# Kernel optimization log

Measured on AMD Instinct MI355X. Metric: run time of the kernel, lower is better.

Reference implementation:

```python
import jax, jax.numpy as jnp
import numpy as np

N_NODES = 100000
N_EDGES = 320000
DIM = 256


def _graph_conv(src, dst, h, W, b):
    # DGL GraphConv, norm='both', in_feats == out_feats (aggregate-then-transform)
    ones = jnp.ones((src.shape[0],), dtype=h.dtype)
    out_deg = jnp.clip(jax.ops.segment_sum(ones, src, num_segments=N_NODES), 1.0)
    in_deg = jnp.clip(jax.ops.segment_sum(ones, dst, num_segments=N_NODES), 1.0)
    h = h * (out_deg ** -0.5)[:, None]          # src-side normalization
    agg = jax.ops.segment_sum(h[src], dst, num_segments=N_NODES)  # SpMM (copy_u, sum)
    agg = agg * (in_deg ** -0.5)[:, None]       # dst-side normalization
    return agg @ W + b


def setup_inputs() -> dict:
    key = jax.random.key(0)
    ks = jax.random.split(key, 7)
    src = jax.random.randint(ks[0], (N_EDGES,), 0, N_NODES, dtype=jnp.int32)
    dst = jax.random.randint(ks[1], (N_EDGES,), 0, N_NODES, dtype=jnp.int32)
    node_feature = jax.random.normal(ks[2], (N_NODES, DIM), dtype=jnp.float32)
    s = 1.0 / np.sqrt(DIM)
    W1 = jax.random.normal(ks[3], (DIM, DIM), dtype=jnp.float32) * s
    b1 = jnp.zeros((DIM,), dtype=jnp.float32)
    W2 = jax.random.normal(ks[4], (DIM, DIM), dtype=jnp.float32) * s
    b2 = jnp.zeros((DIM,), dtype=jnp.float32)
    return {"src": src, "dst": dst, "node_feature": node_feature,
            "W1": W1, "b1": b1, "W2": W2, "b2": b2}


def reference(src, dst, node_feature, W1, b1, W2, b2):
    h = _graph_conv(src, dst, node_feature, W1, b1)
    h = _graph_conv(src, dst, jax.nn.relu(h), W2, b2)
    return jax.nn.relu(h)
```

## Files before the change

kernel.cpp:

```cpp
#include <hip/hip_runtime.h>

#define NN 100000
#define NE 320000
#define DIM 256
#define ELLW 32
#define FEAT_BLKS (NN * DIM / 4 / 256)

typedef _Float16 half8 __attribute__((ext_vector_type(8)));
typedef _Float16 half4v __attribute__((ext_vector_type(4)));
typedef float float4v __attribute__((ext_vector_type(4)));

__global__ void k_build(const int* __restrict__ src, const int* __restrict__ dst,
                        int* __restrict__ cnt_out, int* __restrict__ cnt_in,
                        int* __restrict__ ell) {
    int e = blockIdx.x * 256 + threadIdx.x;
    if (e < NE) {
        int s = src[e], d = dst[e];
        atomicAdd(&cnt_out[s], 1);
        int slot = atomicAdd(&cnt_in[d], 1);
        if (slot < ELLW) ell[d * ELLW + slot] = s;
    }
}

__global__ __launch_bounds__(256)
void k_prep(const float* __restrict__ feat, const int* __restrict__ cnt_out,
            _Float16* __restrict__ fh,
            const float* __restrict__ W1, const float* __restrict__ W2,
            _Float16* __restrict__ WT1, _Float16* __restrict__ WT2) {
    int b = blockIdx.x;
    if (b < FEAT_BLKS) {
        int i = b * 256 + threadIdx.x;
        int row = i >> 6;
        float w = rsqrtf(fmaxf((float)cnt_out[row], 1.f));
        float4 v = reinterpret_cast<const float4*>(feat)[i];
        half4v o;
        o[0] = (_Float16)(v.x * w); o[1] = (_Float16)(v.y * w);
        o[2] = (_Float16)(v.z * w); o[3] = (_Float16)(v.w * w);
        reinterpret_cast<half4v*>(fh)[i] = o;
    } else {
        int i = (b - FEAT_BLKS) * 256 + threadIdx.x;
        int k = i >> 8, n = i & 255;
        WT1[(size_t)n * DIM + k] = (_Float16)W1[(size_t)k * DIM + n];
        WT2[(size_t)n * DIM + k] = (_Float16)W2[(size_t)k * DIM + n];
    }
}

__global__ __launch_bounds__(256)
void k_gather(const int* __restrict__ deg, const int* __restrict__ ell,
              const _Float16* __restrict__ feat, _Float16* __restrict__ agg) {
    const int t = threadIdx.x, lane = t & 63;
    const int half = lane >> 5, sl = lane & 31;
    const int d = blockIdx.x * 4 + (t >> 6);
    if (d >= NN) return;
    const int c = sl << 3;
    const size_t e0 = (size_t)d * ELLW;
    const int dg = deg[d];
    int myidx = (lane < 16) ? ell[e0 + lane] : 0;
    const int cap = min(dg, ELLW);
    float acc[8] = {};

#define GATHER_ROUND(E0)                                                      \
    {                                                                         \
        bool pa = (E0) + half < cap, pb = (E0) + 2 + half < cap;              \
        int  sa = __shfl(myidx, (E0) + half);                                 \
        int  sb = __shfl(myidx, (E0) + 2 + half);                             \
        half8 va = {}, vb = {};                                               \
        if (pa) va = *reinterpret_cast<const half8*>(feat + (size_t)sa * DIM + c); \
        if (pb) vb = *reinterpret_cast<const half8*>(feat + (size_t)sb * DIM + c); \
        _Pragma("unroll")                                                     \
        for (int q = 0; q < 8; ++q) acc[q] += (float)va[q] + (float)vb[q];    \
    }

    if (cap > 0)  GATHER_ROUND(0)
    if (cap > 4)  GATHER_ROUND(4)
    if (cap > 8)  GATHER_ROUND(8)
    if (cap > 12) GATHER_ROUND(12)
#undef GATHER_ROUND
    for (int e = 16 + half; e < cap; e += 2) {
        int s = ell[e0 + e];
        half8 v = *reinterpret_cast<const half8*>(feat + (size_t)s * DIM + c);
        #pragma unroll
        for (int q = 0; q < 8; ++q) acc[q] += (float)v[q];
    }

    #pragma unroll
    for (int q = 0; q < 8; ++q) acc[q] += __shfl_xor(acc[q], 32);
    if (half == 0) {
        half8 o;
        #pragma unroll
        for (int q = 0; q < 8; ++q) o[q] = (_Float16)acc[q];
        *reinterpret_cast<half8*>(agg + (size_t)d * DIM + c) = o;
    }
}

#define LDA 40

template <typename OutT, bool PRESCALE>
__global__ __launch_bounds__(256)
void k_gemm(const _Float16* __restrict__ A, const _Float16* __restrict__ WT,
            const float* __restrict__ bias,
            const int* __restrict__ cnt_in, const int* __restrict__ cnt_out,
            OutT* __restrict__ out) {
    __shared__ _Float16 As[64 * LDA];

    const int t    = threadIdx.x;
    const int lane = t & 63;
    const int wn   = t >> 6;
    const int l15  = lane & 15, quad = lane >> 4;
    const int bm   = blockIdx.x * 64;

    const int sr = t >> 2, sc = t & 3;
    const _Float16* aptr = A + (size_t)(bm + sr) * DIM + sc * 8;
    const _Float16* bp[4];
    #pragma unroll
    for (int nt = 0; nt < 4; ++nt)
        bp[nt] = WT + (size_t)(wn * 64 + nt * 16 + l15) * DIM + quad * 8;

    float4v acc[4][4] = {};
    half8 sv = *reinterpret_cast<const half8*>(aptr);

    for (int k0 = 0; k0 < DIM; k0 += 32) {
        half8 bf[4];
        #pragma unroll
        for (int nt = 0; nt < 4; ++nt)
            bf[nt] = *reinterpret_cast<const half8*>(bp[nt] + k0);

        *reinterpret_cast<half8*>(&As[sr * LDA + sc * 8]) = sv;
        __syncthreads();

        if (k0 + 32 < DIM)
            sv = *reinterpret_cast<const half8*>(aptr + k0 + 32);

        half8 af[4];
        #pragma unroll
        for (int mt = 0; mt < 4; ++mt)
            af[mt] = *reinterpret_cast<half8*>(&As[(mt * 16 + l15) * LDA + quad * 8]);

        #pragma unroll
        for (int mt = 0; mt < 4; ++mt)
            #pragma unroll
            for (int nt = 0; nt < 4; ++nt)
                acc[mt][nt] = __builtin_amdgcn_mfma_f32_16x16x32_f16(af[mt], bf[nt], acc[mt][nt], 0, 0, 0);
        __syncthreads();
    }

    const int colb = wn * 64;
    float bcol[4];
    #pragma unroll
    for (int nt = 0; nt < 4; ++nt)
        bcol[nt] = bias[colb + nt * 16 + l15];

    #pragma unroll
    for (int mt = 0; mt < 4; ++mt) {
        #pragma unroll
        for (int r = 0; r < 4; ++r) {
            int row = bm + mt * 16 + quad * 4 + r;
            if (row < NN) {
                float s  = rsqrtf(fmaxf((float)cnt_in[row], 1.f));
                float ps = PRESCALE ? rsqrtf(fmaxf((float)cnt_out[row], 1.f)) : 1.0f;
                #pragma unroll
                for (int nt = 0; nt < 4; ++nt) {
                    int col = colb + nt * 16 + l15;
                    float v = fmaxf(acc[mt][nt][r] * s + bcol[nt], 0.f) * ps;
                    out[(size_t)row * DIM + col] = (OutT)v;
                }
            }
        }
    }
}

extern "C" void kernel_launch(void* const* d_in, const int* in_sizes, int n_in,
                              void* d_out, int out_size, void* d_ws, size_t ws_size,
                              hipStream_t stream) {
    const int*   src  = (const int*)d_in[0];
    const int*   dst  = (const int*)d_in[1];
    const float* feat = (const float*)d_in[2];
    const float* W1   = (const float*)d_in[3];
    const float* b1   = (const float*)d_in[4];
    const float* W2   = (const float*)d_in[5];
    const float* b2   = (const float*)d_in[6];
    float* out = (float*)d_out;

    int*      cnt_out = (int*)d_ws;
    int*      cnt_in  = cnt_out + NN;
    int*      ell     = cnt_in + NN;
    _Float16* WT1     = (_Float16*)(ell + (size_t)NN * ELLW);
    _Float16* WT2     = WT1 + DIM * DIM;
    _Float16* fh      = WT2 + DIM * DIM;

    _Float16* agg1 = (_Float16*)d_out;
    _Float16* h1   = agg1 + (size_t)NN * DIM;
    _Float16* agg2 = fh;

    hipMemsetAsync(d_ws, 0, (size_t)2 * NN * sizeof(int), stream);

    k_build<<<(NE + 255) / 256, 256, 0, stream>>>(src, dst, cnt_out, cnt_in, ell);
    k_prep <<<FEAT_BLKS + 256, 256, 0, stream>>>(feat, cnt_out, fh, W1, W2, WT1, WT2);

    const int ggrid = (NN + 63) / 64;

    k_gather<<<(NN + 3) / 4, 256, 0, stream>>>(cnt_in, ell, fh, agg1);
    k_gemm<_Float16, true><<<ggrid, 256, 0, stream>>>(agg1, WT1, b1, cnt_in, cnt_out, h1);

    k_gather<<<(NN + 3) / 4, 256, 0, stream>>>(cnt_in, ell, h1, agg2);
    k_gemm<float, false><<<ggrid, 256, 0, stream>>>(agg2, WT2, b2, cnt_in, cnt_out, out);
}
```

Measured before the change: 389.8 us.

## Fuse neighbor gather with MFMA GEMM, staging aggregated rows in LDS

Merges the ELL gather and the GEMM into one kernel per layer. Each block gathers its 64 destination rows into a full-K LDS tile, then runs the MFMA GEMM straight from shared memory. This drops the global write and re-read of the aggregated fp16 feature matrices and two launches. In exchange, each wave gathers 16 rows one after another, and the larger LDS tile may lower occupancy and hide less gather latency.

```diff
diff --git a/kernel.cpp b/kernel.cpp
--- a/kernel.cpp
+++ b/kernel.cpp
@@ -45,19 +45,36 @@
     }
 }
 
+#define LDA 264
+
+template <typename OutT, bool PRESCALE>
 __global__ __launch_bounds__(256)
-void k_gather(const int* __restrict__ deg, const int* __restrict__ ell,
-              const _Float16* __restrict__ feat, _Float16* __restrict__ agg) {
-    const int t = threadIdx.x, lane = t & 63;
+void k_fused(const int* __restrict__ deg, const int* __restrict__ ell,
+             const _Float16* __restrict__ T,
+             const _Float16* __restrict__ WT,
+             const float* __restrict__ bias,
+             const int* __restrict__ cnt_in, const int* __restrict__ cnt_out,
+             OutT* __restrict__ out) {
+    __shared__ _Float16 As[64 * LDA];
+
+    const int t    = threadIdx.x;
+    const int lane = t & 63;
+    const int w    = t >> 6;
     const int half = lane >> 5, sl = lane & 31;
-    const int d = blockIdx.x * 4 + (t >> 6);
-    if (d >= NN) return;
-    const int c = sl << 3;
-    const size_t e0 = (size_t)d * ELLW;
-    const int dg = deg[d];
-    int myidx = (lane < 16) ? ell[e0 + lane] : 0;
-    const int cap = min(dg, ELLW);
-    float acc[8] = {};
+    const int bm   = blockIdx.x * 64;
+    const int c    = sl << 3;
+
+    int dgv = (lane < 16) ? deg[bm + w * 16 + lane] : 0;
+
+    for (int i = 0; i < 16; ++i) {
+        const int r = w * 16 + i;
+        const int d = bm + r;
+        float acc[8] = {};
+        if (d < NN) {
+            const size_t e0 = (size_t)d * ELLW;
+            const int dg  = __shfl(dgv, i);
+            const int cap = min(dg, ELLW);
+            int myidx = (lane < 16) ? ell[e0 + lane] : 0;
 
 #define GATHER_ROUND(E0)                                                      \
     {                                                                         \
@@ -65,86 +82,58 @@
         int  sa = __shfl(myidx, (E0) + half);                                 \
         int  sb = __shfl(myidx, (E0) + 2 + half);                             \
         half8 va = {}, vb = {};                                               \
-        if (pa) va = *reinterpret_cast<const half8*>(feat + (size_t)sa * DIM + c); \
-        if (pb) vb = *reinterpret_cast<const half8*>(feat + (size_t)sb * DIM + c); \
+        if (pa) va = *reinterpret_cast<const half8*>(T + (size_t)sa * DIM + c); \
+        if (pb) vb = *reinterpret_cast<const half8*>(T + (size_t)sb * DIM + c); \
         _Pragma("unroll")                                                     \
         for (int q = 0; q < 8; ++q) acc[q] += (float)va[q] + (float)vb[q];    \
     }
+            if (cap > 0)  GATHER_ROUND(0)
+            if (cap > 4)  GATHER_ROUND(4)
+            if (cap > 8)  GATHER_ROUND(8)
+            if (cap > 12) GATHER_ROUND(12)
+#undef GATHER_ROUND
+            for (int e = 16 + half; e < cap; e += 2) {
+                int s = ell[e0 + e];
+                half8 v = *reinterpret_cast<const half8*>(T + (size_t)s * DIM + c);
+                #pragma unroll
+                for (int q = 0; q < 8; ++q) acc[q] += (float)v[q];
+            }
+        }
+        #pragma unroll
+        for (int q = 0; q < 8; ++q) acc[q] += __shfl_xor(acc[q], 32);
+        if (half == 0) {
+            half8 o;
+            #pragma unroll
+            for (int q = 0; q < 8; ++q) o[q] = (_Float16)acc[q];
+            *reinterpret_cast<half8*>(&As[r * LDA + c]) = o;
+        }
+    }
+    __syncthreads();
 
-    if (cap > 0)  GATHER_ROUND(0)
-    if (cap > 4)  GATHER_ROUND(4)
-    if (cap > 8)  GATHER_ROUND(8)
-    if (cap > 12) GATHER_ROUND(12)
-#undef GATHER_ROUND
-    for (int e = 16 + half; e < cap; e += 2) {
-        int s = ell[e0 + e];
-        half8 v = *reinterpret_cast<const half8*>(feat + (size_t)s * DIM + c);
-        #pragma unroll
-        for (int q = 0; q < 8; ++q) acc[q] += (float)v[q];
-    }
-
-    #pragma unroll
-    for (int q = 0; q < 8; ++q) acc[q] += __shfl_xor(acc[q], 32);
-    if (half == 0) {
-        half8 o;
-        #pragma unroll
-        for (int q = 0; q < 8; ++q) o[q] = (_Float16)acc[q];
-        *reinterpret_cast<half8*>(agg + (size_t)d * DIM + c) = o;
-    }
-}
-
-#define LDA 40
-
-template <typename OutT, bool PRESCALE>
-__global__ __launch_bounds__(256)
-void k_gemm(const _Float16* __restrict__ A, const _Float16* __restrict__ WT,
-            const float* __restrict__ bias,
-            const int* __restrict__ cnt_in, const int* __restrict__ cnt_out,
-            OutT* __restrict__ out) {
-    __shared__ _Float16 As[64 * LDA];
-
-    const int t    = threadIdx.x;
-    const int lane = t & 63;
-    const int wn   = t >> 6;
-    const int l15  = lane & 15, quad = lane >> 4;
-    const int bm   = blockIdx.x * 64;
-
-    const int sr = t >> 2, sc = t & 3;
-    const _Float16* aptr = A + (size_t)(bm + sr) * DIM + sc * 8;
+    const int l15 = lane & 15, quad = lane >> 4;
     const _Float16* bp[4];
     #pragma unroll
     for (int nt = 0; nt < 4; ++nt)
-        bp[nt] = WT + (size_t)(wn * 64 + nt * 16 + l15) * DIM + quad * 8;
+        bp[nt] = WT + (size_t)(w * 64 + nt * 16 + l15) * DIM + quad * 8;
 
-    float4v acc[4][4] = {};
-    half8 sv = *reinterpret_cast<const half8*>(aptr);
-
+    float4v acc4[4][4] = {};
     for (int k0 = 0; k0 < DIM; k0 += 32) {
         half8 bf[4];
         #pragma unroll
         for (int nt = 0; nt < 4; ++nt)
             bf[nt] = *reinterpret_cast<const half8*>(bp[nt] + k0);
-
-        *reinterpret_cast<half8*>(&As[sr * LDA + sc * 8]) = sv;
-        __syncthreads();
-
-        if (k0 + 32 < DIM)
-            sv = *reinterpret_cast<const half8*>(aptr + k0 + 32);
-
         half8 af[4];
         #pragma unroll
         for (int mt = 0; mt < 4; ++mt)
-            af[mt] = *reinterpret_cast<half8*>(&As[(mt * 16 + l15) * LDA + quad * 8]);
-
+            af[mt] = *reinterpret_cast<half8*>(&As[(mt * 16 + l15) * LDA + quad * 8 + k0]);
         #pragma unroll
         for (int mt = 0; mt < 4; ++mt)
             #pragma unroll
             for (int nt = 0; nt < 4; ++nt)
-                acc[mt][nt] = __builtin_amdgcn_mfma_f32_16x16x32_f16(af[mt], bf[nt], acc[mt][nt], 0, 0, 0);
-        __syncthreads();
+                acc4[mt][nt] = __builtin_amdgcn_mfma_f32_16x16x32_f16(af[mt], bf[nt], acc4[mt][nt], 0, 0, 0);
     }
 
-    const int colb = wn * 64;
+    const int colb = w * 64;
     float bcol[4];
     #pragma unroll
     for (int nt = 0; nt < 4; ++nt)
@@ -161,7 +150,7 @@
                 #pragma unroll
                 for (int nt = 0; nt < 4; ++nt) {
                     int col = colb + nt * 16 + l15;
-                    float v = fmaxf(acc[mt][nt][r] * s + bcol[nt], 0.f) * ps;
+                    float v = fmaxf(acc4[mt][nt][r] * s + bcol[nt], 0.f) * ps;
                     out[(size_t)row * DIM + col] = (OutT)v;
                 }
             }
@@ -187,10 +176,7 @@
     _Float16* WT1     = (_Float16*)(ell + (size_t)NN * ELLW);
     _Float16* WT2     = WT1 + DIM * DIM;
     _Float16* fh      = WT2 + DIM * DIM;
-
-    _Float16* agg1 = (_Float16*)d_out;
-    _Float16* h1   = agg1 + (size_t)NN * DIM;
-    _Float16* agg2 = fh;
+    _Float16* h1      = fh + (size_t)NN * DIM;
 
     hipMemsetAsync(d_ws, 0, (size_t)2 * NN * sizeof(int), stream);
 
@@ -199,9 +185,6 @@
 
     const int ggrid = (NN + 63) / 64;
 
-    k_gather<<<(NN + 3) / 4, 256, 0, stream>>>(cnt_in, ell, fh, agg1);
-    k_gemm<_Float16, true><<<ggrid, 256, 0, stream>>>(agg1, WT1, b1, cnt_in, cnt_out, h1);
-
-    k_gather<<<(NN + 3) / 4, 256, 0, stream>>>(cnt_in, ell, h1, agg2);
-    k_gemm<float, false><<<ggrid, 256, 0, stream>>>(agg2, WT2, b2, cnt_in, cnt_out, out);
+    k_fused<_Float16, true ><<<ggrid, 256, 0, stream>>>(cnt_in, ell, fh, WT1, b1, cnt_in, cnt_out, h1);
+    k_fused<float,    false><<<ggrid, 256, 0, stream>>>(cnt_in, ell, h1, WT2, b2, cnt_in, cnt_out, out);
 }
```

Result: slower. 414.5 us (+6.3%).
